# Kernel optimization log

Measured on AMD Instinct MI355X. Metric: run time of the kernel, lower is better.

## Reference

```python
import jax, jax.numpy as jnp
import numpy as np

EPS = 1e-10

def _log_scaling(feats):
    # feats: (N, 15) raw attributes
    lshape = jnp.sqrt(feats[:, 7:8]) / (jnp.sqrt(feats[:, 6:7]) + EPS)  # sqrt(pca_small)/sqrt(pca_big)
    cosangle = jnp.cos(feats[:, 5:6])
    sinangle = jnp.sin(feats[:, 5:6])
    logged = jnp.log(jnp.abs(feats[:, 5:]) + EPS)  # cols 5..14 logged
    # drop logged angle (col 5), keep logged cols 6..14
    return jnp.concatenate([feats[:, :5], logged[:, 1:], lshape, cosangle, sinangle], axis=1)  # (N,17)


def setup_inputs() -> dict:
    rng = np.random.RandomState(0)
    N = 2 ** 21          # number of maxtree components
    H = W = 4096         # image size
    # parent pointers: sorted tree, parent[i] < i; root (node 0) marked -1
    parent = (rng.rand(N) * np.maximum(np.arange(N), 1)).astype(np.int32)
    parent[0] = -1
    # per-node gray-level increment w.r.t. parent
    diff = rng.randn(N).astype(np.float32)
    # raw attributes (N,15): positive-ish geometry stats, angle in col 5
    attributes = (rng.rand(N, 15).astype(np.float32) * 10.0 + 0.1)
    attributes[:, 5] = rng.rand(N).astype(np.float32) * 2.0 * np.pi  # angle
    pixel_node = rng.randint(0, N, size=(H, W)).astype(np.int32)
    weight = (rng.rand(17, 1).astype(np.float32) - 0.5) * 0.02  # uniform(-0.01,0.01)
    bias = np.zeros((1,), dtype=np.float32)
    return {
        "maxtree_diff": jnp.asarray(diff),
        "attributes": jnp.asarray(attributes),
        "weight": jnp.asarray(weight),
        "bias": jnp.asarray(bias),
        "maxtree_parent": jnp.asarray(parent),
        "pixel_node": jnp.asarray(pixel_node),
    }


def reference(maxtree_diff, attributes, weight, bias, maxtree_parent, pixel_node):
    N = maxtree_diff.shape[0]
    rescaled = _log_scaling(attributes)                      # (N,17)
    linear = rescaled @ weight + bias[None, :]               # (N,1)
    cc_scores = jax.nn.sigmoid(linear)[:, 0]                 # (N,)
    term = maxtree_diff * cc_scores                          # (N,) per-node contribution
    # ancestor-chain prefix sum via pointer doubling; sentinel node N has term 0
    par = jnp.where(maxtree_parent < 0, N, maxtree_parent)
    term_ext = jnp.concatenate([term, jnp.zeros((1,), term.dtype)])
    par_ext = jnp.concatenate([par, jnp.array([N], dtype=par.dtype)])
    steps = int(np.ceil(np.log2(N)))
    for _ in range(steps):
        term_ext = term_ext + term_ext[par_ext]
        par_ext = par_ext[par_ext]
    node_vals = term_ext[:N]                                 # filtered gray value per node
    return node_vals[pixel_node]                             # (H,W)
```

## Files before the change

### kernel.cpp

```cpp
#include <hip/hip_runtime.h>
#include <math.h>

#define EPSF 1e-10f

typedef int   vi4 __attribute__((ext_vector_type(4)));
typedef float vf4 __attribute__((ext_vector_type(4)));

struct Pair { float term; int parent; };

__device__ __forceinline__ unsigned short f32_to_bf16(float f) {
    unsigned int u = __float_as_uint(f);
    u += 0x7fffu + ((u >> 16) & 1u);
    return (unsigned short)(u >> 16);
}
__device__ __forceinline__ float bf16_to_f32(unsigned short h) {
    return __uint_as_float(((unsigned int)h) << 16);
}

__global__ __launch_bounds__(256) void term_kernel(
    const float* __restrict__ diff,
    const float* __restrict__ attr,
    const float* __restrict__ weight,
    const float* __restrict__ bias,
    const int*   __restrict__ parent,
    Pair* __restrict__ pairs, int N)
{
    int i = blockIdx.x * blockDim.x + threadIdx.x;
    if (i >= N) return;
    const float* a = attr + (long long)i * 15;
    float f[15];
#pragma unroll
    for (int k = 0; k < 15; ++k) f[k] = a[k];

    float acc = bias[0];
#pragma unroll
    for (int k = 0; k < 5; ++k) acc += f[k] * weight[k];
#pragma unroll
    for (int k = 0; k < 9; ++k)
        acc += logf(fabsf(f[6 + k]) + EPSF) * weight[5 + k];
    acc += (sqrtf(f[7]) / (sqrtf(f[6]) + EPSF)) * weight[14];
    acc += cosf(f[5]) * weight[15];
    acc += sinf(f[5]) * weight[16];

    float sig = 1.0f / (1.0f + expf(-acc));
    Pair pr; pr.term = diff[i] * sig; pr.parent = parent[i];
    pairs[i] = pr;
}

__global__ __launch_bounds__(256) void chain_phase(
    const Pair* __restrict__ pairs,
    float* __restrict__ nv,
    unsigned short* __restrict__ nvb,
    int lo, int hi)
{
    int i = lo + blockIdx.x * blockDim.x + threadIdx.x;
    if (i >= hi) return;
    float s = 0.0f;
    int j = i;
    while (j >= lo) {
        Pair pr = pairs[j];
        s += pr.term;
        j = pr.parent;
    }
    if (j >= 0) s += nv[j];
    nv[i] = s;
    __builtin_nontemporal_store(f32_to_bf16(s), nvb + i);
}

__global__ __launch_bounds__(256) void gather_kernel(
    const unsigned short* __restrict__ nvb,
    const int* __restrict__ pixel_node,
    float* __restrict__ out, long long M)
{
    long long idx = (long long)blockIdx.x * blockDim.x + threadIdx.x;
    long long stride = (long long)gridDim.x * blockDim.x;
    long long M4 = M >> 2;
    const vi4* pn4 = (const vi4*)pixel_node;
    vf4* out4 = (vf4*)out;

    long long t = idx;
    for (; t + 3 * stride < M4; t += 4 * stride) {
        vi4 p0 = __builtin_nontemporal_load(pn4 + t);
        vi4 p1 = __builtin_nontemporal_load(pn4 + t + stride);
        vi4 p2 = __builtin_nontemporal_load(pn4 + t + 2 * stride);
        vi4 p3 = __builtin_nontemporal_load(pn4 + t + 3 * stride);

        unsigned short g00 = nvb[p0.x], g01 = nvb[p0.y], g02 = nvb[p0.z], g03 = nvb[p0.w];
        unsigned short g10 = nvb[p1.x], g11 = nvb[p1.y], g12 = nvb[p1.z], g13 = nvb[p1.w];
        unsigned short g20 = nvb[p2.x], g21 = nvb[p2.y], g22 = nvb[p2.z], g23 = nvb[p2.w];
        unsigned short g30 = nvb[p3.x], g31 = nvb[p3.y], g32 = nvb[p3.z], g33 = nvb[p3.w];

        vf4 v0, v1, v2, v3;
        v0.x = bf16_to_f32(g00); v0.y = bf16_to_f32(g01);
        v0.z = bf16_to_f32(g02); v0.w = bf16_to_f32(g03);
        v1.x = bf16_to_f32(g10); v1.y = bf16_to_f32(g11);
        v1.z = bf16_to_f32(g12); v1.w = bf16_to_f32(g13);
        v2.x = bf16_to_f32(g20); v2.y = bf16_to_f32(g21);
        v2.z = bf16_to_f32(g22); v2.w = bf16_to_f32(g23);
        v3.x = bf16_to_f32(g30); v3.y = bf16_to_f32(g31);
        v3.z = bf16_to_f32(g32); v3.w = bf16_to_f32(g33);

        __builtin_nontemporal_store(v0, out4 + t);
        __builtin_nontemporal_store(v1, out4 + t + stride);
        __builtin_nontemporal_store(v2, out4 + t + 2 * stride);
        __builtin_nontemporal_store(v3, out4 + t + 3 * stride);
    }
    for (; t < M4; t += stride) {
        vi4 p = __builtin_nontemporal_load(pn4 + t);
        vf4 v;
        v.x = bf16_to_f32(nvb[p.x]);
        v.y = bf16_to_f32(nvb[p.y]);
        v.z = bf16_to_f32(nvb[p.z]);
        v.w = bf16_to_f32(nvb[p.w]);
        __builtin_nontemporal_store(v, out4 + t);
    }
    for (long long s = (M4 << 2) + idx; s < M; s += stride)
        out[s] = bf16_to_f32(nvb[pixel_node[s]]);
}

extern "C" void kernel_launch(void* const* d_in, const int* in_sizes, int n_in,
                              void* d_out, int out_size, void* d_ws, size_t ws_size,
                              hipStream_t stream) {
    const float* diff   = (const float*)d_in[0];
    const float* attr   = (const float*)d_in[1];
    const float* weight = (const float*)d_in[2];
    const float* bias   = (const float*)d_in[3];
    const int*   parent = (const int*)d_in[4];
    const int*   pixel  = (const int*)d_in[5];
    float* out = (float*)d_out;

    int N = in_sizes[0];
    Pair*           pairs = (Pair*)d_ws;
    float*          nv    = (float*)(pairs + N);
    unsigned short* nvb   = (unsigned short*)(nv + N);

    int T1 = N < (1 << 16) ? N : (1 << 16);
    int T2 = N < (1 << 20) ? N : (1 << 20);

    int blocks = (N + 255) / 256;
    term_kernel<<<blocks, 256, 0, stream>>>(diff, attr, weight, bias, parent, pairs, N);

    chain_phase<<<(T1 + 255) / 256, 256, 0, stream>>>(pairs, nv, nvb, 0, T1);
    if (T2 > T1)
        chain_phase<<<(T2 - T1 + 255) / 256, 256, 0, stream>>>(pairs, nv, nvb, T1, T2);
    if (N > T2)
        chain_phase<<<(N - T2 + 255) / 256, 256, 0, stream>>>(pairs, nv, nvb, T2, N);

    gather_kernel<<<4096, 256, 0, stream>>>(nvb, pixel, out, (long long)out_size);
}
```

Before: 365.3 us.

## Use fast math intrinsics and nontemporal loads for random gathers

Result: slower. 558.4 us (+52.8%).

```diff
diff --git a/kernel.cpp b/kernel.cpp
--- a/kernel.cpp
+++ b/kernel.cpp
@@ -5,6 +5,7 @@
 
 typedef int   vi4 __attribute__((ext_vector_type(4)));
 typedef float vf4 __attribute__((ext_vector_type(4)));
+typedef int   vi2 __attribute__((ext_vector_type(2)));
 
 struct Pair { float term; int parent; };
 
@@ -37,12 +38,12 @@
     for (int k = 0; k < 5; ++k) acc += f[k] * weight[k];
 #pragma unroll
     for (int k = 0; k < 9; ++k)
-        acc += logf(fabsf(f[6 + k]) + EPSF) * weight[5 + k];
-    acc += (sqrtf(f[7]) / (sqrtf(f[6]) + EPSF)) * weight[14];
-    acc += cosf(f[5]) * weight[15];
-    acc += sinf(f[5]) * weight[16];
+        acc += __logf(fabsf(f[6 + k]) + EPSF) * weight[5 + k];
+    acc += __fdividef(sqrtf(f[7]), sqrtf(f[6]) + EPSF) * weight[14];
+    acc += __cosf(f[5]) * weight[15];
+    acc += __sinf(f[5]) * weight[16];
 
-    float sig = 1.0f / (1.0f + expf(-acc));
+    float sig = 1.0f / (1.0f + __expf(-acc));
     Pair pr; pr.term = diff[i] * sig; pr.parent = parent[i];
     pairs[i] = pr;
 }
@@ -57,12 +58,13 @@
     if (i >= hi) return;
     float s = 0.0f;
     int j = i;
+    const vi2* p2 = (const vi2*)pairs;
     while (j >= lo) {
-        Pair pr = pairs[j];
-        s += pr.term;
-        j = pr.parent;
+        vi2 pr = __builtin_nontemporal_load(p2 + j);
+        s += __int_as_float(pr.x);
+        j = pr.y;
     }
-    if (j >= 0) s += nv[j];
+    if (j >= 0) s += __builtin_nontemporal_load(nv + j);
     nv[i] = s;
     __builtin_nontemporal_store(f32_to_bf16(s), nvb + i);
 }
@@ -85,10 +87,22 @@
         vi4 p2 = __builtin_nontemporal_load(pn4 + t + 2 * stride);
         vi4 p3 = __builtin_nontemporal_load(pn4 + t + 3 * stride);
 
-        unsigned short g00 = nvb[p0.x], g01 = nvb[p0.y], g02 = nvb[p0.z], g03 = nvb[p0.w];
-        unsigned short g10 = nvb[p1.x], g11 = nvb[p1.y], g12 = nvb[p1.z], g13 = nvb[p1.w];
-        unsigned short g20 = nvb[p2.x], g21 = nvb[p2.y], g22 = nvb[p2.z], g23 = nvb[p2.w];
-        unsigned short g30 = nvb[p3.x], g31 = nvb[p3.y], g32 = nvb[p3.z], g33 = nvb[p3.w];
+        unsigned short g00 = __builtin_nontemporal_load(nvb + p0.x);
+        unsigned short g01 = __builtin_nontemporal_load(nvb + p0.y);
+        unsigned short g02 = __builtin_nontemporal_load(nvb + p0.z);
+        unsigned short g03 = __builtin_nontemporal_load(nvb + p0.w);
+        unsigned short g10 = __builtin_nontemporal_load(nvb + p1.x);
+        unsigned short g11 = __builtin_nontemporal_load(nvb + p1.y);
+        unsigned short g12 = __builtin_nontemporal_load(nvb + p1.z);
+        unsigned short g13 = __builtin_nontemporal_load(nvb + p1.w);
+        unsigned short g20 = __builtin_nontemporal_load(nvb + p2.x);
+        unsigned short g21 = __builtin_nontemporal_load(nvb + p2.y);
+        unsigned short g22 = __builtin_nontemporal_load(nvb + p2.z);
+        unsigned short g23 = __builtin_nontemporal_load(nvb + p2.w);
+        unsigned short g30 = __builtin_nontemporal_load(nvb + p3.x);
+        unsigned short g31 = __builtin_nontemporal_load(nvb + p3.y);
+        unsigned short g32 = __builtin_nontemporal_load(nvb + p3.z);
+        unsigned short g33 = __builtin_nontemporal_load(nvb + p3.w);
 
         vf4 v0, v1, v2, v3;
         v0.x = bf16_to_f32(g00); v0.y = bf16_to_f32(g01);
@@ -108,14 +122,14 @@
     for (; t < M4; t += stride) {
         vi4 p = __builtin_nontemporal_load(pn4 + t);
         vf4 v;
-        v.x = bf16_to_f32(nvb[p.x]);
-        v.y = bf16_to_f32(nvb[p.y]);
-        v.z = bf16_to_f32(nvb[p.z]);
-        v.w = bf16_to_f32(nvb[p.w]);
+        v.x = bf16_to_f32(__builtin_nontemporal_load(nvb + p.x));
+        v.y = bf16_to_f32(__builtin_nontemporal_load(nvb + p.y));
+        v.z = bf16_to_f32(__builtin_nontemporal_load(nvb + p.z));
+        v.w = bf16_to_f32(__builtin_nontemporal_load(nvb + p.w));
         __builtin_nontemporal_store(v, out4 + t);
     }
     for (long long s = (M4 << 2) + idx; s < M; s += stride)
-        out[s] = bf16_to_f32(nvb[pixel_node[s]]);
+        out[s] = bf16_to_f32(__builtin_nontemporal_load(nvb + pixel_node[s]));
 }
 
 extern "C" void kernel_launch(void* const* d_in, const int* in_sizes, int n_in,
```
